# Kernel optimization log

Hardware: AMD Instinct MI355X
Metric: run time of the kernel (lower is better)

## Reference

```python
import jax, jax.numpy as jnp
import numpy as np

B, T, F, E = 256, 256, 8, 128
H = 2 * E  # hidden_dim = 2*embedding_dim = 256
NL = 5     # num_layers per LSTM stack


def setup_inputs() -> dict:
    key = jax.random.key(0)
    ks = jax.random.split(key, 9)
    s1 = 1.0 / np.sqrt(H)
    s2 = 1.0 / np.sqrt(E)
    u = lambda k, shape, s: jax.random.uniform(k, shape, jnp.float32, -s, s)
    return {
        "x": jax.random.normal(ks[0], (B, T, F), jnp.float32),
        # stack 1: input F -> hidden H, 5 layers. b = b_ih + b_hh combined.
        "w_ih0_1": u(ks[1], (4 * H, F), s1),
        "w_ihr_1": u(ks[2], (NL - 1, 4 * H, H), s1),
        "w_hh_1": u(ks[3], (NL, 4 * H, H), s1),
        "b_1": u(ks[4], (NL, 4 * H), s1),
        # stack 2: input H -> hidden E, 5 layers
        "w_ih0_2": u(ks[5], (4 * E, H), s2),
        "w_ihr_2": u(ks[6], (NL - 1, 4 * E, E), s2),
        "w_hh_2": u(ks[7], (NL, 4 * E, E), s2),
        "b_2": u(ks[8], (NL, 4 * E), s2),
    }


def _lstm_layer(x, w_ih, w_hh, b):
    """x: [B,T,D] -> (outputs [B,T,Hd], final hidden [B,Hd]). PyTorch gate order i,f,g,o."""
    Hd = w_hh.shape[-1]
    # precompute input contribution for all timesteps (the big GEMM)
    xg = jnp.einsum('btd,gd->tbg', x, w_ih) + b  # [T,B,4Hd]
    h0 = jnp.zeros((x.shape[0], Hd), x.dtype)

    def step(carry, xt):
        h, c = carry
        g = xt + h @ w_hh.T
        i, f, gg, o = jnp.split(g, 4, axis=-1)
        c = jax.nn.sigmoid(f) * c + jax.nn.sigmoid(i) * jnp.tanh(gg)
        h = jax.nn.sigmoid(o) * jnp.tanh(c)
        return (h, c), h

    (h, _), hs = jax.lax.scan(step, (h0, h0), xg)
    return jnp.swapaxes(hs, 0, 1), h


def _stack(x, w_ih0, w_ihr, w_hh, b):
    y, h = _lstm_layer(x, w_ih0, w_hh[0], b[0])
    for l in range(1, w_hh.shape[0]):
        y, h = _lstm_layer(y, w_ihr[l - 1], w_hh[l], b[l])
    return y, h


def reference(x, w_ih0_1, w_ihr_1, w_hh_1, b_1, w_ih0_2, w_ihr_2, w_hh_2, b_2):
    x = x.reshape(x.shape[0], T, F)
    y, _ = _stack(x, w_ih0_1, w_ihr_1, w_hh_1, b_1)   # [B,T,H]
    _, h = _stack(y, w_ih0_2, w_ihr_2, w_hh_2, b_2)   # h: [B,E] last layer final hidden
    return h
```

## Files before the change

### kernel.cpp

```cpp
#include <hip/hip_runtime.h>
#include <math.h>

typedef unsigned short u16;
typedef unsigned int   u32;
typedef unsigned long long u64;
typedef __bf16 bf16x8 __attribute__((ext_vector_type(8)));
typedef float  f32x4  __attribute__((ext_vector_type(4)));

#define BB 256
#define TT 256
#define HD 256
#define ED 128
#define DEPTH 4
#define NE 137

#define H_U32   (10 * DEPTH * BB * HD)
#define CTR_OFF H_U32
#define GRP_OFF (CTR_OFF + 512)
#define XP_OFF  (GRP_OFF + 640)
#define XP_U32  (BB * TT * 8)
#define WT_OFF  (XP_OFF + XP_U32)

__constant__ size_t g_woff[10] = {0ul,589824ul,1638400ul,2686976ul,3735552ul,
                                  4784128ul,5177344ul,5439488ul,5701632ul,5963776ul};
__constant__ int g_cb[11] = {0,73728,204800,335872,466944,598016,
                             647168,679936,712704,745472,778240};

__device__ __forceinline__ u16 f2bf_hi(float f) {
    u32 u = __float_as_uint(f);
    u32 r = (u + 0x7FFFu + ((u >> 16) & 1u)) >> 16;
    return (u16)r;
}
__device__ __forceinline__ float bf2f(u16 h) { return __uint_as_float(((u32)h) << 16); }
__device__ __forceinline__ float sigmoidf_(float v) { return 1.0f / (1.0f + expf(-v)); }

__global__ __launch_bounds__(256) void zero_state(u32* wsd) {
    const int n = XP_OFF;
    for (int i = blockIdx.x * blockDim.x + threadIdx.x; i < n; i += gridDim.x * blockDim.x)
        wsd[i] = 0u;
}

__global__ __launch_bounds__(256) void conv_x(const float* __restrict__ x, u32* __restrict__ wsd) {
    u32* xp = wsd + XP_OFF;
    for (int i = blockIdx.x * blockDim.x + threadIdx.x; i < XP_U32; i += gridDim.x * blockDim.x) {
        float v = x[i];
        u16 hi = f2bf_hi(v);
        u16 lo = f2bf_hi(v - bf2f(hi));
        xp[i] = (u32)hi | ((u32)lo << 16);
    }
}

__global__ __launch_bounds__(256) void conv_all(
    const float* __restrict__ w_ih0_1, const float* __restrict__ w_ihr_1,
    const float* __restrict__ w_hh_1,
    const float* __restrict__ w_ih0_2, const float* __restrict__ w_ihr_2,
    const float* __restrict__ w_hh_2,
    u32* __restrict__ wsd)
{
    __bf16* dst0 = (__bf16*)(wsd + WT_OFF);
    const int nch = 778240;
    for (int ci = blockIdx.x * blockDim.x + threadIdx.x; ci < nch;
         ci += gridDim.x * blockDim.x) {
        int l = 0;
        while (ci >= g_cb[l + 1]) ++l;
        int di = ci - g_cb[l];

        const int hd  = (l < 5) ? 256 : 128;
        const int din = (l == 0) ? 32 : ((l < 6) ? 256 : 128);
        const int xw  = (l == 0) ? 8 : din;
        const int Kp  = din + hd;
        const int nk  = Kp >> 5;

        const float *wih, *whh; int wihld, whhld;
        if (l == 0)      { wih = w_ih0_1;                                whh = w_hh_1;
                           wihld = 8;   whhld = 256; }
        else if (l < 5)  { wih = w_ihr_1 + (size_t)(l - 1) * 1024 * 256; whh = w_hh_1 + (size_t)l * 1024 * 256;
                           wihld = 256; whhld = 256; }
        else if (l == 5) { wih = w_ih0_2;                                whh = w_hh_2;
                           wihld = 256; whhld = 128; }
        else             { wih = w_ihr_2 + (size_t)(l - 6) * 512 * 128;  whh = w_hh_2 + (size_t)(l - 5) * 512 * 128;
                           wihld = 128; whhld = 128; }

        int lane = di & 63;
        int rem  = di >> 6;
        int kt   = rem % nk;
        int rem2 = rem / nk;
        int p    = rem2 & 1;
        int g    = (rem2 >> 1) & 3;
        int jt   = rem2 >> 3;
        int r15  = lane & 15, kq = lane >> 4;
        int row  = g * hd + jt * 16 + r15;

        bf16x8 o8;
        #pragma unroll
        for (int e = 0; e < 8; ++e) {
            int k = kt * 32 + kq * 8 + e;
            float v = 0.0f;
            if (k < xw) v = wih[(size_t)row * wihld + k];
            else if (k >= din && k < Kp) v = whh[(size_t)row * whhld + (k - din)];
            __bf16 h = (__bf16)v;
            o8[e] = p ? (__bf16)(v - (float)h) : h;
        }
        *(bf16x8*)(dst0 + g_woff[l] + (size_t)di * 8) = o8;
    }
}

__device__ __forceinline__ void unpack8(const uint4& a, const uint4& b, bf16x8& bh, bf16x8& bl) {
    union { u32 u[4]; bf16x8 v; } H, L;
    H.u[0] = (a.x & 0xFFFFu) | (a.y << 16);
    H.u[1] = (a.z & 0xFFFFu) | (a.w << 16);
    H.u[2] = (b.x & 0xFFFFu) | (b.y << 16);
    H.u[3] = (b.z & 0xFFFFu) | (b.w << 16);
    L.u[0] = (a.x >> 16) | (a.y & 0xFFFF0000u);
    L.u[1] = (a.z >> 16) | (a.w & 0xFFFF0000u);
    L.u[2] = (b.x >> 16) | (b.y & 0xFFFF0000u);
    L.u[3] = (b.z >> 16) | (b.w & 0xFFFF0000u);
    bh = H.v; bl = L.v;
}

template<int NKI, int NKT, bool ISL0>
__device__ void run_persist(int l, int bid, int xcd, int jt, int bt, int hd, u32 arr7,
    int nblkg, u32* __restrict__ gflg,
    const float* __restrict__ bias, u32* __restrict__ hbuf, u32* __restrict__ ctr,
    const u32* __restrict__ xp, float* __restrict__ out, const u16* __restrict__ A_sh)
{
    constexpr int DIN = NKI * 32;
    constexpr int RS  = (NKT < 4) ? NKT : 4;

    const int tid  = threadIdx.x;
    const int lane = tid & 63;
    const int wv   = tid >> 6;
    const int r15  = lane & 15;
    const int kqc  = lane >> 4;
    const int brow = bt * 128 + wv * 16 + r15;
    const int j0   = jt * 16 + kqc * 4;

    float bgr[4][4];
    #pragma unroll
    for (int g = 0; g < 4; ++g) {
        float4 v = *(const float4*)&bias[g * hd + j0];
        bgr[g][0] = v.x; bgr[g][1] = v.y; bgr[g][2] = v.z; bgr[g][3] = v.w;
    }

    int offH[4], offL[4];
    #pragma unroll
    for (int g = 0; g < 4; ++g) {
        offH[g] = (g * 2)     * NKT * 512 + lane * 8;
        offL[g] = (g * 2 + 1) * NKT * 512 + lane * 8;
    }

    float4 cv = make_float4(0.f, 0.f, 0.f, 0.f);
    const int lm = (l > 0) ? (l - 1) : 0;

    auto STEP = [&](int t) {
        const u32* hin   = hbuf + ((size_t)lm * DEPTH + (t & 3)) * (BB * HD);
        const u32* hprev = hbuf + ((size_t)l * DEPTH + ((t - 1) & 3)) * (BB * HD);
        u32*       hout  = hbuf + ((size_t)l * DEPTH + (t & 3)) * (BB * HD);

        auto ldB = [&](int kt, uint4& A, uint4& B) {
            if constexpr (ISL0) {
                if (kt == 0) {
                    if (kqc == 0) {
                        const uint4* p = (const uint4*)(xp + ((size_t)brow * TT + t) * 8);
                        A = p[0]; B = p[1];
                    } else { A = make_uint4(0,0,0,0); B = make_uint4(0,0,0,0); }
                } else {
                    const u32* p = hprev + (size_t)brow * HD + (kt * 32 - 32) + kqc * 8;
                    A = *(const uint4*)p; B = *(const uint4*)(p + 4);
                }
            } else {
                const int k0 = kt * 32 + kqc * 8;
                const u32* p = (k0 < DIN) ? (hin + (size_t)brow * HD + k0)
                                          : (hprev + (size_t)brow * HD + (k0 - DIN));
                A = *(const uint4*)p; B = *(const uint4*)(p + 4);
            }
        };

        f32x4 acc0 = {0.f,0.f,0.f,0.f}, acc1 = {0.f,0.f,0.f,0.f};
        f32x4 acc2 = {0.f,0.f,0.f,0.f}, acc3 = {0.f,0.f,0.f,0.f};

        uint4 ra[RS], rb[RS];
        #pragma unroll
        for (int i = 0; i < RS; ++i) ldB(i, ra[i], rb[i]);

        #pragma unroll
        for (int kt = 0; kt < NKT; ++kt) {
            bf16x8 bh, bl;
            unpack8(ra[kt % RS], rb[kt % RS], bh, bl);
            if (kt + RS < NKT) ldB(kt + RS, ra[kt % RS], rb[kt % RS]);

            const int kof = kt * 512;
            bf16x8 a0h = *(const bf16x8*)&A_sh[offH[0] + kof];
            bf16x8 a1h = *(const bf16x8*)&A_sh[offH[1] + kof];
            bf16x8 a2h = *(const bf16x8*)&A_sh[offH[2] + kof];
            bf16x8 a3h = *(const bf16x8*)&A_sh[offH[3] + kof];
            bf16x8 a0l = *(const bf16x8*)&A_sh[offL[0] + kof];
            bf16x8 a1l = *(const bf16x8*)&A_sh[offL[1] + kof];
            bf16x8 a2l = *(const bf16x8*)&A_sh[offL[2] + kof];
            bf16x8 a3l = *(const bf16x8*)&A_sh[offL[3] + kof];

            acc0 = __builtin_amdgcn_mfma_f32_16x16x32_bf16(a0h, bh, acc0, 0, 0, 0);
            acc1 = __builtin_amdgcn_mfma_f32_16x16x32_bf16(a1h, bh, acc1, 0, 0, 0);
            acc2 = __builtin_amdgcn_mfma_f32_16x16x32_bf16(a2h, bh, acc2, 0, 0, 0);
            acc3 = __builtin_amdgcn_mfma_f32_16x16x32_bf16(a3h, bh, acc3, 0, 0, 0);
            acc0 = __builtin_amdgcn_mfma_f32_16x16x32_bf16(a0h, bl, acc0, 0, 0, 0);
            acc1 = __builtin_amdgcn_mfma_f32_16x16x32_bf16(a1h, bl, acc1, 0, 0, 0);
            acc2 = __builtin_amdgcn_mfma_f32_16x16x32_bf16(a2h, bl, acc2, 0, 0, 0);
            acc3 = __builtin_amdgcn_mfma_f32_16x16x32_bf16(a3h, bl, acc3, 0, 0, 0);
            acc0 = __builtin_amdgcn_mfma_f32_16x16x32_bf16(a0l, bh, acc0, 0, 0, 0);
            acc1 = __builtin_amdgcn_mfma_f32_16x16x32_bf16(a1l, bh, acc1, 0, 0, 0);
            acc2 = __builtin_amdgcn_mfma_f32_16x16x32_bf16(a2l, bh, acc2, 0, 0, 0);
            acc3 = __builtin_amdgcn_mfma_f32_16x16x32_bf16(a3l, bh, acc3, 0, 0, 0);
        }

        float4 hv;
        {
            float i_, f_, g_, o_;
            i_ = sigmoidf_(acc0[0] + bgr[0][0]); f_ = sigmoidf_(acc1[0] + bgr[1][0]);
            g_ = tanhf   (acc2[0] + bgr[2][0]); o_ = sigmoidf_(acc3[0] + bgr[3][0]);
            cv.x = fmaf(f_, cv.x, i_ * g_); hv.x = o_ * tanhf(cv.x);
            i_ = sigmoidf_(acc0[1] + bgr[0][1]); f_ = sigmoidf_(acc1[1] + bgr[1][1]);
            g_ = tanhf   (acc2[1] + bgr[2][1]); o_ = sigmoidf_(acc3[1] + bgr[3][1]);
            cv.y = fmaf(f_, cv.y, i_ * g_); hv.y = o_ * tanhf(cv.y);
            i_ = sigmoidf_(acc0[2] + bgr[0][2]); f_ = sigmoidf_(acc1[2] + bgr[1][2]);
            g_ = tanhf   (acc2[2] + bgr[2][2]); o_ = sigmoidf_(acc3[2] + bgr[3][2]);
            cv.z = fmaf(f_, cv.z, i_ * g_); hv.z = o_ * tanhf(cv.z);
            i_ = sigmoidf_(acc0[3] + bgr[0][3]); f_ = sigmoidf_(acc1[3] + bgr[1][3]);
            g_ = tanhf   (acc2[3] + bgr[2][3]); o_ = sigmoidf_(acc3[3] + bgr[3][3]);
            cv.w = fmaf(f_, cv.w, i_ * g_); hv.w = o_ * tanhf(cv.w);
        }

        u32 pk0, pk1, pk2, pk3;
        {
            u16 h0 = f2bf_hi(hv.x); pk0 = (u32)h0 | ((u32)f2bf_hi(hv.x - bf2f(h0)) << 16);
            u16 h1 = f2bf_hi(hv.y); pk1 = (u32)h1 | ((u32)f2bf_hi(hv.y - bf2f(h1)) << 16);
            u16 h2 = f2bf_hi(hv.z); pk2 = (u32)h2 | ((u32)f2bf_hi(hv.z - bf2f(h2)) << 16);
            u16 h3 = f2bf_hi(hv.w); pk3 = (u32)h3 | ((u32)f2bf_hi(hv.w - bf2f(h3)) << 16);
        }
        u64* hp = (u64*)(hout + (size_t)brow * HD + j0);
        __hip_atomic_store(hp + 0, (u64)pk0 | ((u64)pk1 << 32), __ATOMIC_RELAXED, __HIP_MEMORY_SCOPE_AGENT);
        __hip_atomic_store(hp + 1, (u64)pk2 | ((u64)pk3 << 32), __ATOMIC_RELAXED, __HIP_MEMORY_SCOPE_AGENT);

        if (l == 9 && t == TT - 1)
            *(float4*)&out[(size_t)brow * ED + j0] = hv;
    };

    for (int E = 0; E < NE; ++E) {
        const int t0 = 2 * (E - l);
        if (t0 >= 0 && t0 < TT) {
            STEP(t0);
            __syncthreads();
            if (tid == 0)
                __hip_atomic_fetch_add(gflg, 1u, __ATOMIC_RELAXED, __HIP_MEMORY_SCOPE_AGENT);
        }
        const int t1 = t0 + 1;
        if (t1 >= 1 && t1 < TT) {
            if (tid == 0) {
                const u32 tg = (u32)nblkg * (u32)(E - l + 1);
                for (int it = 0; it < (1 << 20); ++it) {
                    if (__hip_atomic_load(gflg, __ATOMIC_RELAXED,
                                          __HIP_MEMORY_SCOPE_AGENT) >= tg) break;
                    __builtin_amdgcn_s_sleep(1);
                }
            }
            __syncthreads();
            STEP(t1);
        }

        __syncthreads();
        if (tid == 0) {
            __hip_atomic_fetch_add(&ctr[xcd * 32], 1u,
                                   __ATOMIC_RELAXED, __HIP_MEMORY_SCOPE_AGENT);
            const u32 w1 = (u32)(E + 1);
            if (bid == 0) {
                for (int it = 0; it < (1 << 22); ++it) {
                    bool ok = true;
                    #pragma unroll
                    for (int r = 0; r < 8; ++r) {
                        u32 tgt = ((r == 7) ? arr7 : 32u) * w1;
                        ok &= (__hip_atomic_load(&ctr[r * 32], __ATOMIC_RELAXED,
                                                 __HIP_MEMORY_SCOPE_AGENT) >= tgt);
                    }
                    if (ok) break;
                    __builtin_amdgcn_s_sleep(1);
                }
                __hip_atomic_store(&ctr[256], w1, __ATOMIC_RELAXED, __HIP_MEMORY_SCOPE_AGENT);
            } else {
                for (int it = 0; it < (1 << 22); ++it) {
                    if (__hip_atomic_load(&ctr[256], __ATOMIC_RELAXED,
                                          __HIP_MEMORY_SCOPE_AGENT) >= w1) break;
                    __builtin_amdgcn_s_sleep(1);
                }
            }
            __builtin_amdgcn_fence(__ATOMIC_ACQUIRE, "agent");
        }
        __syncthreads();
    }
}

__global__ __launch_bounds__(512, 2) void lstm_persist(
    const float* __restrict__ b_1, const float* __restrict__ b_2,
    u32* __restrict__ wsd, float* __restrict__ out)
{
    __shared__ __align__(16) u16 A_sh[65536];

    const int bid = blockIdx.x;
    const int xcd = bid & 7, slot = bid >> 3;
    int l, jt, bt;
    if (xcd < 5)      { l = xcd;               bt = slot >> 4;        jt = slot & 15; }
    else if (xcd == 5){ l = 5 + (slot >> 4);   bt = (slot >> 3) & 1;  jt = slot & 7; }
    else if (xcd == 6){ l = 7 + (slot >> 4);   bt = (slot >> 3) & 1;  jt = slot & 7; }
    else              { if (slot >= 16) return; l = 9; bt = slot >> 3; jt = slot & 7; }

    const int hd  = (l < 5) ? 256 : 128;
    const int din = (l == 0) ? 32 : ((l < 6) ? 256 : 128);
    const int nk  = (din + hd) >> 5;
    const float* bias = (l < 5) ? (b_1 + l * 1024) : (b_2 + (l - 5) * 512);
    const int nblkg = (l < 5) ? 32 : 16;

    u32* hbuf = wsd;
    u32* ctr  = wsd + CTR_OFF;
    u32* gflg = wsd + GRP_OFF + (size_t)(l * 2 + bt) * 32;
    const u32* xp = wsd + XP_OFF;
    const u16* wt = (const u16*)(wsd + WT_OFF);

    const int ng = (l < 5) ? 16 : 8;
    (void)nblkg;

    {
        const uint4* src = (const uint4*)(wt + g_woff[l] + (size_t)jt * 8 * nk * 512);
        uint4* dst = (uint4*)A_sh;
        const int n4 = nk * 512;
        for (int i = threadIdx.x; i < n4; i += 512) dst[i] = src[i];
    }
    __syncthreads();

    if (l == 0)
        run_persist<1, 9, true >(l, bid, xcd, jt, bt, hd, 16u, ng, gflg, bias, hbuf, ctr, xp, out, A_sh);
    else if (l < 5)
        run_persist<8, 16, false>(l, bid, xcd, jt, bt, hd, 16u, ng, gflg, bias, hbuf, ctr, xp, out, A_sh);
    else if (l == 5)
        run_persist<8, 12, false>(l, bid, xcd, jt, bt, hd, 16u, ng, gflg, bias, hbuf, ctr, xp, out, A_sh);
    else
        run_persist<4, 8, false>(l, bid, xcd, jt, bt, hd, 16u, ng, gflg, bias, hbuf, ctr, xp, out, A_sh);
}

extern "C" void kernel_launch(void* const* d_in, const int* in_sizes, int n_in,
                              void* d_out, int out_size, void* d_ws, size_t ws_size,
                              hipStream_t stream) {
    const float* x       = (const float*)d_in[0];
    const float* w_ih0_1 = (const float*)d_in[1];
    const float* w_ihr_1 = (const float*)d_in[2];
    const float* w_hh_1  = (const float*)d_in[3];
    const float* b_1     = (const float*)d_in[4];
    const float* w_ih0_2 = (const float*)d_in[5];
    const float* w_ihr_2 = (const float*)d_in[6];
    const float* w_hh_2  = (const float*)d_in[7];
    const float* b_2     = (const float*)d_in[8];
    u32*   wsd = (u32*)d_ws;
    float* out = (float*)d_out;

    hipLaunchKernelGGL(zero_state, dim3(1024), dim3(256), 0, stream, wsd);
    hipLaunchKernelGGL(conv_all, dim3(1024), dim3(256), 0, stream,
                       w_ih0_1, w_ihr_1, w_hh_1, w_ih0_2, w_ihr_2, w_hh_2, wsd);
    hipLaunchKernelGGL(conv_x, dim3(256), dim3(256), 0, stream, x, wsd);
    hipLaunchKernelGGL(lstm_persist, dim3(256), dim3(512), 0, stream,
                       b_1, b_2, wsd, out);
}
```

Before: 2.998 ms.

## Process four timesteps per global epoch and keep part of the weights in registers

The wavefront schedule changes from two timesteps per grid-wide barrier to four, with intra-group flag waits between steps. This halves the number of epochs and deepens the hidden-state ring buffer to eight slots. The high-precision halves of gates 0 and 1 now live in registers, loaded directly from global memory, so the shared-memory weight slice shrinks to six sub-blocks and fewer LDS reads are issued per k-tile. The prefetch depth drops from four to three to make room. The cost is heavy register pressure from NKT-sized register arrays, which may spill or limit occupancy, and longer per-epoch dependency chains across layers.

Result: slower. 3.197 ms (+6.6%).

```diff
diff --git a/kernel.cpp b/kernel.cpp
--- a/kernel.cpp
+++ b/kernel.cpp
@@ -11,8 +11,8 @@
 #define TT 256
 #define HD 256
 #define ED 128
-#define DEPTH 4
-#define NE 137
+#define DEPTH 8
+#define NE 73
 
 #define H_U32   (10 * DEPTH * BB * HD)
 #define CTR_OFF H_U32
@@ -120,12 +120,13 @@
 
 template<int NKI, int NKT, bool ISL0>
 __device__ void run_persist(int l, int bid, int xcd, int jt, int bt, int hd, u32 arr7,
-    int nblkg, u32* __restrict__ gflg,
+    int ng, u32* __restrict__ gflg,
     const float* __restrict__ bias, u32* __restrict__ hbuf, u32* __restrict__ ctr,
-    const u32* __restrict__ xp, float* __restrict__ out, const u16* __restrict__ A_sh)
+    const u32* __restrict__ xp, float* __restrict__ out,
+    const u16* __restrict__ A_sh, const u16* __restrict__ wslice)
 {
     constexpr int DIN = NKI * 32;
-    constexpr int RS  = (NKT < 4) ? NKT : 4;
+    constexpr int RS  = (NKT < 3) ? NKT : 3;
 
     const int tid  = threadIdx.x;
     const int lane = tid & 63;
@@ -135,6 +136,13 @@
     const int brow = bt * 128 + wv * 16 + r15;
     const int j0   = jt * 16 + kqc * 4;
 
+    bf16x8 A_reg[2][NKT];
+    #pragma unroll
+    for (int g = 0; g < 2; ++g)
+        #pragma unroll
+        for (int kt = 0; kt < NKT; ++kt)
+            A_reg[g][kt] = *(const bf16x8*)(wslice + ((size_t)(g * 2) * NKT + kt) * 512 + lane * 8);
+
     float bgr[4][4];
     #pragma unroll
     for (int g = 0; g < 4; ++g) {
@@ -142,20 +150,19 @@
         bgr[g][0] = v.x; bgr[g][1] = v.y; bgr[g][2] = v.z; bgr[g][3] = v.w;
     }
 
-    int offH[4], offL[4];
+    int loOff[4];
     #pragma unroll
-    for (int g = 0; g < 4; ++g) {
-        offH[g] = (g * 2)     * NKT * 512 + lane * 8;
-        offL[g] = (g * 2 + 1) * NKT * 512 + lane * 8;
-    }
+    for (int g = 0; g < 4; ++g) loOff[g] = (g * NKT) * 512 + lane * 8;
+    const int hi2Off = (4 * NKT) * 512 + lane * 8;
+    const int hi3Off = (5 * NKT) * 512 + lane * 8;
 
     float4 cv = make_float4(0.f, 0.f, 0.f, 0.f);
     const int lm = (l > 0) ? (l - 1) : 0;
 
     auto STEP = [&](int t) {
-        const u32* hin   = hbuf + ((size_t)lm * DEPTH + (t & 3)) * (BB * HD);
-        const u32* hprev = hbuf + ((size_t)l * DEPTH + ((t - 1) & 3)) * (BB * HD);
-        u32*       hout  = hbuf + ((size_t)l * DEPTH + (t & 3)) * (BB * HD);
+        const u32* hin   = hbuf + ((size_t)lm * DEPTH + (t & 7)) * (BB * HD);
+        const u32* hprev = hbuf + ((size_t)l * DEPTH + ((t - 1) & 7)) * (BB * HD);
+        u32*       hout  = hbuf + ((size_t)l * DEPTH + (t & 7)) * (BB * HD);
 
         auto ldB = [&](int kt, uint4& A, uint4& B) {
             if constexpr (ISL0) {
@@ -190,14 +197,14 @@
             if (kt + RS < NKT) ldB(kt + RS, ra[kt % RS], rb[kt % RS]);
 
             const int kof = kt * 512;
-            bf16x8 a0h = *(const bf16x8*)&A_sh[offH[0] + kof];
-            bf16x8 a1h = *(const bf16x8*)&A_sh[offH[1] + kof];
-            bf16x8 a2h = *(const bf16x8*)&A_sh[offH[2] + kof];
-            bf16x8 a3h = *(const bf16x8*)&A_sh[offH[3] + kof];
-            bf16x8 a0l = *(const bf16x8*)&A_sh[offL[0] + kof];
-            bf16x8 a1l = *(const bf16x8*)&A_sh[offL[1] + kof];
-            bf16x8 a2l = *(const bf16x8*)&A_sh[offL[2] + kof];
-            bf16x8 a3l = *(const bf16x8*)&A_sh[offL[3] + kof];
+            bf16x8 a0h = A_reg[0][kt];
+            bf16x8 a1h = A_reg[1][kt];
+            bf16x8 a2h = *(const bf16x8*)&A_sh[hi2Off + kof];
+            bf16x8 a3h = *(const bf16x8*)&A_sh[hi3Off + kof];
+            bf16x8 a0l = *(const bf16x8*)&A_sh[loOff[0] + kof];
+            bf16x8 a1l = *(const bf16x8*)&A_sh[loOff[1] + kof];
+            bf16x8 a2l = *(const bf16x8*)&A_sh[loOff[2] + kof];
+            bf16x8 a3l = *(const bf16x8*)&A_sh[loOff[3] + kof];
 
             acc0 = __builtin_amdgcn_mfma_f32_16x16x32_bf16(a0h, bh, acc0, 0, 0, 0);
             acc1 = __builtin_amdgcn_mfma_f32_16x16x32_bf16(a1h, bh, acc1, 0, 0, 0);
@@ -246,25 +253,29 @@
     };
 
     for (int E = 0; E < NE; ++E) {
-        const int t0 = 2 * (E - l);
-        if (t0 >= 0 && t0 < TT) {
-            STEP(t0);
-            __syncthreads();
-            if (tid == 0)
-                __hip_atomic_fetch_add(gflg, 1u, __ATOMIC_RELAXED, __HIP_MEMORY_SCOPE_AGENT);
-        }
-        const int t1 = t0 + 1;
-        if (t1 >= 1 && t1 < TT) {
-            if (tid == 0) {
-                const u32 tg = (u32)nblkg * (u32)(E - l + 1);
-                for (int it = 0; it < (1 << 20); ++it) {
-                    if (__hip_atomic_load(gflg, __ATOMIC_RELAXED,
-                                          __HIP_MEMORY_SCOPE_AGENT) >= tg) break;
-                    __builtin_amdgcn_s_sleep(1);
+        const int ep = E - l;
+        if (ep >= 0 && ep < 64) {
+            #pragma unroll 1
+            for (int i = 0; i < 4; ++i) {
+                const int t = 4 * ep + i;
+                if (i > 0) {
+                    if (tid == 0) {
+                        const u32 tg = (u32)ng * (u32)(3 * ep + i);
+                        for (int it = 0; it < (1 << 20); ++it) {
+                            if (__hip_atomic_load(gflg, __ATOMIC_RELAXED,
+                                                  __HIP_MEMORY_SCOPE_AGENT) >= tg) break;
+                            __builtin_amdgcn_s_sleep(1);
+                        }
+                    }
+                    __syncthreads();
+                }
+                STEP(t);
+                if (i < 3) {
+                    __syncthreads();
+                    if (tid == 0)
+                        __hip_atomic_fetch_add(gflg, 1u, __ATOMIC_RELAXED, __HIP_MEMORY_SCOPE_AGENT);
                 }
             }
-            __syncthreads();
-            STEP(t1);
         }
 
         __syncthreads();
@@ -302,7 +313,7 @@
     const float* __restrict__ b_1, const float* __restrict__ b_2,
     u32* __restrict__ wsd, float* __restrict__ out)
 {
-    __shared__ __align__(16) u16 A_sh[65536];
+    __shared__ __align__(16) u16 A_sh[49152];
 
     const int bid = blockIdx.x;
     const int xcd = bid & 7, slot = bid >> 3;
@@ -316,33 +327,36 @@
     const int din = (l == 0) ? 32 : ((l < 6) ? 256 : 128);
     const int nk  = (din + hd) >> 5;
     const float* bias = (l < 5) ? (b_1 + l * 1024) : (b_2 + (l - 5) * 512);
-    const int nblkg = (l < 5) ? 32 : 16;
 
     u32* hbuf = wsd;
     u32* ctr  = wsd + CTR_OFF;
     u32* gflg = wsd + GRP_OFF + (size_t)(l * 2 + bt) * 32;
     const u32* xp = wsd + XP_OFF;
     const u16* wt = (const u16*)(wsd + WT_OFF);
+    const u16* wslice = wt + g_woff[l] + (size_t)jt * 8 * nk * 512;
 
     const int ng = (l < 5) ? 16 : 8;
-    (void)nblkg;
 
     {
-        const uint4* src = (const uint4*)(wt + g_woff[l] + (size_t)jt * 8 * nk * 512);
-        uint4* dst = (uint4*)A_sh;
-        const int n4 = nk * 512;
-        for (int i = threadIdx.x; i < n4; i += 512) dst[i] = src[i];
+        const uint4* src4 = (const uint4*)wslice;
+        uint4* dst4 = (uint4*)A_sh;
+        const int spc = nk * 64;
+        for (int i = threadIdx.x; i < 6 * spc; i += 512) {
+            int d = i / spc, r = i - d * spc;
+            int s = (d < 4) ? (d * 2 + 1) : ((d == 4) ? 4 : 6);
+            dst4[i] = src4[s * spc + r];
+        }
     }
     __syncthreads();
 
     if (l == 0)
-        run_persist<1, 9, true >(l, bid, xcd, jt, bt, hd, 16u, ng, gflg, bias, hbuf, ctr, xp, out, A_sh);
+        run_persist<1, 9, true >(l, bid, xcd, jt, bt, hd, 16u, ng, gflg, bias, hbuf, ctr, xp, out, A_sh, wslice);
     else if (l < 5)
-        run_persist<8, 16, false>(l, bid, xcd, jt, bt, hd, 16u, ng, gflg, bias, hbuf, ctr, xp, out, A_sh);
+        run_persist<8, 16, false>(l, bid, xcd, jt, bt, hd, 16u, ng, gflg, bias, hbuf, ctr, xp, out, A_sh, wslice);
     else if (l == 5)
-        run_persist<8, 12, false>(l, bid, xcd, jt, bt, hd, 16u, ng, gflg, bias, hbuf, ctr, xp, out, A_sh);
+        run_persist<8, 12, false>(l, bid, xcd, jt, bt, hd, 16u, ng, gflg, bias, hbuf, ctr, xp, out, A_sh, wslice);
     else
-        run_persist<4, 8, false>(l, bid, xcd, jt, bt, hd, 16u, ng, gflg, bias, hbuf, ctr, xp, out, A_sh);
+        run_persist<4, 8, false>(l, bid, xcd, jt, bt, hd, 16u, ng, gflg, bias, hbuf, ctr, xp, out, A_sh, wslice);
 }
 
 extern "C" void kernel_launch(void* const* d_in, const int* in_sizes, int n_in,
```

## Switch recurrent GEMM to 32x32x16 MFMA with gate-interleaved weight layout

Applied to the files above, without the earlier changes.

Replaces the four 16x16x32 MFMA accumulators per gate with 32x32x16 MFMAs whose output rows interleave the four gates for 8 hidden units. The weight repacking kernel is changed so each 32-row tile holds i,f,g,o for one hidden unit. Each wave now covers 32 batch rows and 8 hidden units, and two accumulators alternate over K steps to break MFMA dependency chains. This cuts LDS A-fragment loads and per-step instruction count, at the cost of larger accumulator register use, narrower scalar 32-bit h stores and a changed load prefetch depth.

New measurement: 5.244 ms. 1.75x slower.

```diff
diff --git a/kernel.cpp b/kernel.cpp
--- a/kernel.cpp
+++ b/kernel.cpp
@@ -6,6 +6,7 @@
 typedef unsigned long long u64;
 typedef __bf16 bf16x8 __attribute__((ext_vector_type(8)));
 typedef float  f32x4  __attribute__((ext_vector_type(4)));
+typedef float  f32x16 __attribute__((ext_vector_type(16)));
 
 #define BB 256
 #define TT 256
@@ -69,7 +70,7 @@
         const int din = (l == 0) ? 32 : ((l < 6) ? 256 : 128);
         const int xw  = (l == 0) ? 8 : din;
         const int Kp  = din + hd;
-        const int nk  = Kp >> 5;
+        const int NK2 = Kp >> 4;
 
         const float *wih, *whh; int wihld, whhld;
         if (l == 0)      { wih = w_ih0_1;                                whh = w_hh_1;
@@ -83,18 +84,20 @@
 
         int lane = di & 63;
         int rem  = di >> 6;
-        int kt   = rem % nk;
-        int rem2 = rem / nk;
+        int s    = rem % NK2;
+        int rem2 = rem / NK2;
         int p    = rem2 & 1;
-        int g    = (rem2 >> 1) & 3;
-        int jt   = rem2 >> 3;
-        int r15  = lane & 15, kq = lane >> 4;
-        int row  = g * hd + jt * 16 + r15;
+        int jh   = (rem2 >> 1) & 1;
+        int jt   = rem2 >> 2;
+        int r31  = lane & 31;
+        int jloc = r31 >> 2, gate = r31 & 3;
+        int kh   = (lane >> 5) * 8;
+        int row  = gate * hd + jt * 16 + jh * 8 + jloc;
 
         bf16x8 o8;
         #pragma unroll
         for (int e = 0; e < 8; ++e) {
-            int k = kt * 32 + kq * 8 + e;
+            int k = s * 16 + kh + e;
             float v = 0.0f;
             if (k < xw) v = wih[(size_t)row * wihld + k];
             else if (k >= din && k < Kp) v = whh[(size_t)row * whhld + (k - din)];
@@ -118,38 +121,37 @@
     bh = H.v; bl = L.v;
 }
 
-template<int NKI, int NKT, bool ISL0>
+template<int DIN16, int NK2, bool ISL0>
 __device__ void run_persist(int l, int bid, int xcd, int jt, int bt, int hd, u32 arr7,
-    int nblkg, u32* __restrict__ gflg,
+    int ng, u32* __restrict__ gflg,
     const float* __restrict__ bias, u32* __restrict__ hbuf, u32* __restrict__ ctr,
     const u32* __restrict__ xp, float* __restrict__ out, const u16* __restrict__ A_sh)
 {
-    constexpr int DIN = NKI * 32;
-    constexpr int RS  = (NKT < 4) ? NKT : 4;
+    constexpr int DIN = DIN16 * 16;
+    constexpr int RS  = (NK2 < 3) ? NK2 : 3;
 
     const int tid  = threadIdx.x;
     const int lane = tid & 63;
     const int wv   = tid >> 6;
-    const int r15  = lane & 15;
-    const int kqc  = lane >> 4;
-    const int brow = bt * 128 + wv * 16 + r15;
-    const int j0   = jt * 16 + kqc * 4;
+    const int bq   = wv >> 1;
+    const int jh   = wv & 1;
+    const int r31  = lane & 31;
+    const int hi   = lane >> 5;
+    const int kh   = hi * 8;
+    const int b    = bt * 128 + bq * 32 + r31;
+    const int jBase = jt * 16 + jh * 8;
+
+    const int hiOff = ((jh * 2 + 0) * NK2) * 512 + lane * 8;
+    const int loOff = ((jh * 2 + 1) * NK2) * 512 + lane * 8;
 
     float bgr[4][4];
     #pragma unroll
-    for (int g = 0; g < 4; ++g) {
-        float4 v = *(const float4*)&bias[g * hd + j0];
-        bgr[g][0] = v.x; bgr[g][1] = v.y; bgr[g][2] = v.z; bgr[g][3] = v.w;
-    }
-
-    int offH[4], offL[4];
-    #pragma unroll
-    for (int g = 0; g < 4; ++g) {
-        offH[g] = (g * 2)     * NKT * 512 + lane * 8;
-        offL[g] = (g * 2 + 1) * NKT * 512 + lane * 8;
-    }
-
-    float4 cv = make_float4(0.f, 0.f, 0.f, 0.f);
+    for (int q = 0; q < 4; ++q)
+        #pragma unroll
+        for (int g = 0; g < 4; ++g)
+            bgr[q][g] = bias[g * hd + jBase + 2 * q + hi];
+
+    f32x4 cv = {0.f, 0.f, 0.f, 0.f};
     const int lm = (l > 0) ? (l - 1) : 0;
 
     auto STEP = [&](int t) {
@@ -157,92 +159,70 @@
         const u32* hprev = hbuf + ((size_t)l * DEPTH + ((t - 1) & 3)) * (BB * HD);
         u32*       hout  = hbuf + ((size_t)l * DEPTH + (t & 3)) * (BB * HD);
 
-        auto ldB = [&](int kt, uint4& A, uint4& B) {
+        auto ldB = [&](int s, uint4& A, uint4& B) {
             if constexpr (ISL0) {
-                if (kt == 0) {
-                    if (kqc == 0) {
-                        const uint4* p = (const uint4*)(xp + ((size_t)brow * TT + t) * 8);
+                if (s == 0) {
+                    if (hi == 0) {
+                        const uint4* p = (const uint4*)(xp + ((size_t)b * TT + t) * 8);
                         A = p[0]; B = p[1];
                     } else { A = make_uint4(0,0,0,0); B = make_uint4(0,0,0,0); }
+                } else if (s == 1) {
+                    A = make_uint4(0,0,0,0); B = make_uint4(0,0,0,0);
                 } else {
-                    const u32* p = hprev + (size_t)brow * HD + (kt * 32 - 32) + kqc * 8;
+                    const u32* p = hprev + (size_t)b * HD + (s * 16 - 32) + kh;
                     A = *(const uint4*)p; B = *(const uint4*)(p + 4);
                 }
             } else {
-                const int k0 = kt * 32 + kqc * 8;
-                const u32* p = (k0 < DIN) ? (hin + (size_t)brow * HD + k0)
-                                          : (hprev + (size_t)brow * HD + (k0 - DIN));
+                const int k0 = s * 16 + kh;
+                const u32* p = (k0 < DIN) ? (hin + (size_t)b * HD + k0)
+                                          : (hprev + (size_t)b * HD + (k0 - DIN));
                 A = *(const uint4*)p; B = *(const uint4*)(p + 4);
             }
         };
 
-        f32x4 acc0 = {0.f,0.f,0.f,0.f}, acc1 = {0.f,0.f,0.f,0.f};
-        f32x4 acc2 = {0.f,0.f,0.f,0.f}, acc3 = {0.f,0.f,0.f,0.f};
+        f32x16 accA, accB;
+        #pragma unroll
+        for (int i = 0; i < 16; ++i) { accA[i] = 0.f; accB[i] = 0.f; }
 
         uint4 ra[RS], rb[RS];
         #pragma unroll
         for (int i = 0; i < RS; ++i) ldB(i, ra[i], rb[i]);
 
         #pragma unroll
-        for (int kt = 0; kt < NKT; ++kt) {
+        for (int s = 0; s < NK2; ++s) {
             bf16x8 bh, bl;
-            unpack8(ra[kt % RS], rb[kt % RS], bh, bl);
-            if (kt + RS < NKT) ldB(kt + RS, ra[kt % RS], rb[kt % RS]);
-
-            const int kof = kt * 512;
-            bf16x8 a0h = *(const bf16x8*)&A_sh[offH[0] + kof];
-            bf16x8 a1h = *(const bf16x8*)&A_sh[offH[1] + kof];
-            bf16x8 a2h = *(const bf16x8*)&A_sh[offH[2] + kof];
-            bf16x8 a3h = *(const bf16x8*)&A_sh[offH[3] + kof];
-            bf16x8 a0l = *(const bf16x8*)&A_sh[offL[0] + kof];
-            bf16x8 a1l = *(const bf16x8*)&A_sh[offL[1] + kof];
-            bf16x8 a2l = *(const bf16x8*)&A_sh[offL[2] + kof];
-            bf16x8 a3l = *(const bf16x8*)&A_sh[offL[3] + kof];
-
-            acc0 = __builtin_amdgcn_mfma_f32_16x16x32_bf16(a0h, bh, acc0, 0, 0, 0);
-            acc1 = __builtin_amdgcn_mfma_f32_16x16x32_bf16(a1h, bh, acc1, 0, 0, 0);
-            acc2 = __builtin_amdgcn_mfma_f32_16x16x32_bf16(a2h, bh, acc2, 0, 0, 0);
-            acc3 = __builtin_amdgcn_mfma_f32_16x16x32_bf16(a3h, bh, acc3, 0, 0, 0);
-            acc0 = __builtin_amdgcn_mfma_f32_16x16x32_bf16(a0h, bl, acc0, 0, 0, 0);
-            acc1 = __builtin_amdgcn_mfma_f32_16x16x32_bf16(a1h, bl, acc1, 0, 0, 0);
-            acc2 = __builtin_amdgcn_mfma_f32_16x16x32_bf16(a2h, bl, acc2, 0, 0, 0);
-            acc3 = __builtin_amdgcn_mfma_f32_16x16x32_bf16(a3h, bl, acc3, 0, 0, 0);
-            acc0 = __builtin_amdgcn_mfma_f32_16x16x32_bf16(a0l, bh, acc0, 0, 0, 0);
-            acc1 = __builtin_amdgcn_mfma_f32_16x16x32_bf16(a1l, bh, acc1, 0, 0, 0);
-            acc2 = __builtin_amdgcn_mfma_f32_16x16x32_bf16(a2l, bh, acc2, 0, 0, 0);
-            acc3 = __builtin_amdgcn_mfma_f32_16x16x32_bf16(a3l, bh, acc3, 0, 0, 0);
-        }
-
-        float4 hv;
-        {
-            float i_, f_, g_, o_;
-            i_ = sigmoidf_(acc0[0] + bgr[0][0]); f_ = sigmoidf_(acc1[0] + bgr[1][0]);
-            g_ = tanhf   (acc2[0] + bgr[2][0]); o_ = sigmoidf_(acc3[0] + bgr[3][0]);
-            cv.x = fmaf(f_, cv.x, i_ * g_); hv.x = o_ * tanhf(cv.x);
-            i_ = sigmoidf_(acc0[1] + bgr[0][1]); f_ = sigmoidf_(acc1[1] + bgr[1][1]);
-            g_ = tanhf   (acc2[1] + bgr[2][1]); o_ = sigmoidf_(acc3[1] + bgr[3][1]);
-            cv.y = fmaf(f_, cv.y, i_ * g_); hv.y = o_ * tanhf(cv.y);
-            i_ = sigmoidf_(acc0[2] + bgr[0][2]); f_ = sigmoidf_(acc1[2] + bgr[1][2]);
-            g_ = tanhf   (acc2[2] + bgr[2][2]); o_ = sigmoidf_(acc3[2] + bgr[3][2]);
-            cv.z = fmaf(f_, cv.z, i_ * g_); hv.z = o_ * tanhf(cv.z);
-            i_ = sigmoidf_(acc0[3] + bgr[0][3]); f_ = sigmoidf_(acc1[3] + bgr[1][3]);
-            g_ = tanhf   (acc2[3] + bgr[2][3]); o_ = sigmoidf_(acc3[3] + bgr[3][3]);
-            cv.w = fmaf(f_, cv.w, i_ * g_); hv.w = o_ * tanhf(cv.w);
-        }
-
-        u32 pk0, pk1, pk2, pk3;
-        {
-            u16 h0 = f2bf_hi(hv.x); pk0 = (u32)h0 | ((u32)f2bf_hi(hv.x - bf2f(h0)) << 16);
-            u16 h1 = f2bf_hi(hv.y); pk1 = (u32)h1 | ((u32)f2bf_hi(hv.y - bf2f(h1)) << 16);
-            u16 h2 = f2bf_hi(hv.z); pk2 = (u32)h2 | ((u32)f2bf_hi(hv.z - bf2f(h2)) << 16);
-            u16 h3 = f2bf_hi(hv.w); pk3 = (u32)h3 | ((u32)f2bf_hi(hv.w - bf2f(h3)) << 16);
-        }
-        u64* hp = (u64*)(hout + (size_t)brow * HD + j0);
-        __hip_atomic_store(hp + 0, (u64)pk0 | ((u64)pk1 << 32), __ATOMIC_RELAXED, __HIP_MEMORY_SCOPE_AGENT);
-        __hip_atomic_store(hp + 1, (u64)pk2 | ((u64)pk3 << 32), __ATOMIC_RELAXED, __HIP_MEMORY_SCOPE_AGENT);
-
-        if (l == 9 && t == TT - 1)
-            *(float4*)&out[(size_t)brow * ED + j0] = hv;
+            unpack8(ra[s % RS], rb[s % RS], bh, bl);
+            if (s + RS < NK2) ldB(s + RS, ra[s % RS], rb[s % RS]);
+
+            bf16x8 ah = *(const bf16x8*)&A_sh[hiOff + s * 512];
+            bf16x8 al = *(const bf16x8*)&A_sh[loOff + s * 512];
+
+            if (s & 1) {
+                accB = __builtin_amdgcn_mfma_f32_32x32x16_bf16(ah, bh, accB, 0, 0, 0);
+                accB = __builtin_amdgcn_mfma_f32_32x32x16_bf16(ah, bl, accB, 0, 0, 0);
+                accB = __builtin_amdgcn_mfma_f32_32x32x16_bf16(al, bh, accB, 0, 0, 0);
+            } else {
+                accA = __builtin_amdgcn_mfma_f32_32x32x16_bf16(ah, bh, accA, 0, 0, 0);
+                accA = __builtin_amdgcn_mfma_f32_32x32x16_bf16(ah, bl, accA, 0, 0, 0);
+                accA = __builtin_amdgcn_mfma_f32_32x32x16_bf16(al, bh, accA, 0, 0, 0);
+            }
+        }
+
+        #pragma unroll
+        for (int q = 0; q < 4; ++q) {
+            float i_ = sigmoidf_(accA[q*4+0] + accB[q*4+0] + bgr[q][0]);
+            float f_ = sigmoidf_(accA[q*4+1] + accB[q*4+1] + bgr[q][1]);
+            float g_ = tanhf   (accA[q*4+2] + accB[q*4+2] + bgr[q][2]);
+            float o_ = sigmoidf_(accA[q*4+3] + accB[q*4+3] + bgr[q][3]);
+            cv[q] = fmaf(f_, cv[q], i_ * g_);
+            float hv = o_ * tanhf(cv[q]);
+            u16 h0 = f2bf_hi(hv);
+            u32 pk = (u32)h0 | ((u32)f2bf_hi(hv - bf2f(h0)) << 16);
+            const int j = jBase + 2 * q + hi;
+            __hip_atomic_store(hout + (size_t)b * HD + j, pk,
+                               __ATOMIC_RELAXED, __HIP_MEMORY_SCOPE_AGENT);
+            if (l == 9 && t == TT - 1) out[(size_t)b * ED + j] = hv;
+        }
     };
 
     for (int E = 0; E < NE; ++E) {
@@ -256,7 +236,7 @@
         const int t1 = t0 + 1;
         if (t1 >= 1 && t1 < TT) {
             if (tid == 0) {
-                const u32 tg = (u32)nblkg * (u32)(E - l + 1);
+                const u32 tg = (u32)ng * (u32)(E - l + 1);
                 for (int it = 0; it < (1 << 20); ++it) {
                     if (__hip_atomic_load(gflg, __ATOMIC_RELAXED,
                                           __HIP_MEMORY_SCOPE_AGENT) >= tg) break;
@@ -314,9 +294,8 @@
 
     const int hd  = (l < 5) ? 256 : 128;
     const int din = (l == 0) ? 32 : ((l < 6) ? 256 : 128);
-    const int nk  = (din + hd) >> 5;
+    const int NK2 = (din + hd) >> 4;
     const float* bias = (l < 5) ? (b_1 + l * 1024) : (b_2 + (l - 5) * 512);
-    const int nblkg = (l < 5) ? 32 : 16;
 
     u32* hbuf = wsd;
     u32* ctr  = wsd + CTR_OFF;
@@ -325,24 +304,23 @@
     const u16* wt = (const u16*)(wsd + WT_OFF);
 
     const int ng = (l < 5) ? 16 : 8;
-    (void)nblkg;
 
     {
-        const uint4* src = (const uint4*)(wt + g_woff[l] + (size_t)jt * 8 * nk * 512);
+        const uint4* src = (const uint4*)(wt + g_woff[l] + (size_t)jt * 4 * NK2 * 512);
         uint4* dst = (uint4*)A_sh;
-        const int n4 = nk * 512;
+        const int n4 = NK2 * 256;
         for (int i = threadIdx.x; i < n4; i += 512) dst[i] = src[i];
     }
     __syncthreads();
 
     if (l == 0)
-        run_persist<1, 9, true >(l, bid, xcd, jt, bt, hd, 16u, ng, gflg, bias, hbuf, ctr, xp, out, A_sh);
+        run_persist<2, 18, true >(l, bid, xcd, jt, bt, hd, 16u, ng, gflg, bias, hbuf, ctr, xp, out, A_sh);
     else if (l < 5)
+        run_persist<16, 32, false>(l, bid, xcd, jt, bt, hd, 16u, ng, gflg, bias, hbuf, ctr, xp, out, A_sh);
+    else if (l == 5)
+        run_persist<16, 24, false>(l, bid, xcd, jt, bt, hd, 16u, ng, gflg, bias, hbuf, ctr, xp, out, A_sh);
+    else
         run_persist<8, 16, false>(l, bid, xcd, jt, bt, hd, 16u, ng, gflg, bias, hbuf, ctr, xp, out, A_sh);
-    else if (l == 5)
-        run_persist<8, 12, false>(l, bid, xcd, jt, bt, hd, 16u, ng, gflg, bias, hbuf, ctr, xp, out, A_sh);
-    else
-        run_persist<4, 8, false>(l, bid, xcd, jt, bt, hd, 16u, ng, gflg, bias, hbuf, ctr, xp, out, A_sh);
 }
 
 extern "C" void kernel_launch(void* const* d_in, const int* in_sizes, int n_in,
```

## Split hidden-state ring into hi/lo planes and process four timesteps per epoch

Applied to the files above, without the earlier changes.

Stores the bf16 hi and lo parts of hidden states and the input in separate planes, so loads feed the MFMA operands directly with no unpack shuffles. The ring depth goes from 4 to 8 and each wavefront epoch now covers four timesteps instead of two. This halves the number of global cross-layer barrier epochs (from 137 to 73) and relies more on per-group flags inside an epoch. The cost is more ring memory and longer pipeline fill and drain across layers.

Result: faster. 2.890 ms (-3.6%).

```diff
diff --git a/kernel.cpp b/kernel.cpp
--- a/kernel.cpp
+++ b/kernel.cpp
@@ -11,15 +11,16 @@
 #define TT 256
 #define HD 256
 #define ED 128
-#define DEPTH 4
-#define NE 137
-
-#define H_U32   (10 * DEPTH * BB * HD)
-#define CTR_OFF H_U32
+#define DEPTH 8
+#define NE 73
+
+#define HRING   (10 * DEPTH * BB * HD / 2)
+#define CTR_OFF (2 * HRING)
 #define GRP_OFF (CTR_OFF + 512)
-#define XP_OFF  (GRP_OFF + 640)
-#define XP_U32  (BB * TT * 8)
-#define WT_OFF  (XP_OFF + XP_U32)
+#define XP_U32  (BB * TT * 8 / 2)
+#define XPH_OFF (GRP_OFF + 640)
+#define XPL_OFF (XPH_OFF + XP_U32)
+#define WT_OFF  (XPL_OFF + XP_U32)
 
 __constant__ size_t g_woff[10] = {0ul,589824ul,1638400ul,2686976ul,3735552ul,
                                   4784128ul,5177344ul,5439488ul,5701632ul,5963776ul};
@@ -35,18 +36,20 @@
 __device__ __forceinline__ float sigmoidf_(float v) { return 1.0f / (1.0f + expf(-v)); }
 
 __global__ __launch_bounds__(256) void zero_state(u32* wsd) {
-    const int n = XP_OFF;
+    const int n = XPH_OFF;
     for (int i = blockIdx.x * blockDim.x + threadIdx.x; i < n; i += gridDim.x * blockDim.x)
         wsd[i] = 0u;
 }
 
 __global__ __launch_bounds__(256) void conv_x(const float* __restrict__ x, u32* __restrict__ wsd) {
-    u32* xp = wsd + XP_OFF;
-    for (int i = blockIdx.x * blockDim.x + threadIdx.x; i < XP_U32; i += gridDim.x * blockDim.x) {
+    u16* xph = (u16*)(wsd + XPH_OFF);
+    u16* xpl = (u16*)(wsd + XPL_OFF);
+    const int n = BB * TT * 8;
+    for (int i = blockIdx.x * blockDim.x + threadIdx.x; i < n; i += gridDim.x * blockDim.x) {
         float v = x[i];
         u16 hi = f2bf_hi(v);
-        u16 lo = f2bf_hi(v - bf2f(hi));
-        xp[i] = (u32)hi | ((u32)lo << 16);
+        xph[i] = hi;
+        xpl[i] = f2bf_hi(v - bf2f(hi));
     }
 }
 
@@ -105,27 +108,19 @@
     }
 }
 
-__device__ __forceinline__ void unpack8(const uint4& a, const uint4& b, bf16x8& bh, bf16x8& bl) {
-    union { u32 u[4]; bf16x8 v; } H, L;
-    H.u[0] = (a.x & 0xFFFFu) | (a.y << 16);
-    H.u[1] = (a.z & 0xFFFFu) | (a.w << 16);
-    H.u[2] = (b.x & 0xFFFFu) | (b.y << 16);
-    H.u[3] = (b.z & 0xFFFFu) | (b.w << 16);
-    L.u[0] = (a.x >> 16) | (a.y & 0xFFFF0000u);
-    L.u[1] = (a.z >> 16) | (a.w & 0xFFFF0000u);
-    L.u[2] = (b.x >> 16) | (b.y & 0xFFFF0000u);
-    L.u[3] = (b.z >> 16) | (b.w & 0xFFFF0000u);
-    bh = H.v; bl = L.v;
-}
-
 template<int NKI, int NKT, bool ISL0>
 __device__ void run_persist(int l, int bid, int xcd, int jt, int bt, int hd, u32 arr7,
-    int nblkg, u32* __restrict__ gflg,
-    const float* __restrict__ bias, u32* __restrict__ hbuf, u32* __restrict__ ctr,
-    const u32* __restrict__ xp, float* __restrict__ out, const u16* __restrict__ A_sh)
+    int ng, u32* __restrict__ gflg,
+    const float* __restrict__ bias, u32* __restrict__ wsd, u32* __restrict__ ctr,
+    float* __restrict__ out, const u16* __restrict__ A_sh)
 {
     constexpr int DIN = NKI * 32;
     constexpr int RS  = (NKT < 4) ? NKT : 4;
+
+    u16* hhi = (u16*)wsd;
+    u16* hlo = (u16*)(wsd + HRING);
+    const u16* xph = (const u16*)(wsd + XPH_OFF);
+    const u16* xpl = (const u16*)(wsd + XPL_OFF);
 
     const int tid  = threadIdx.x;
     const int lane = tid & 63;
@@ -153,26 +148,29 @@
     const int lm = (l > 0) ? (l - 1) : 0;
 
     auto STEP = [&](int t) {
-        const u32* hin   = hbuf + ((size_t)lm * DEPTH + (t & 3)) * (BB * HD);
-        const u32* hprev = hbuf + ((size_t)l * DEPTH + ((t - 1) & 3)) * (BB * HD);
-        u32*       hout  = hbuf + ((size_t)l * DEPTH + (t & 3)) * (BB * HD);
-
-        auto ldB = [&](int kt, uint4& A, uint4& B) {
+        const size_t sIn   = ((size_t)lm * DEPTH + (t & 7)) * (BB * HD);
+        const size_t sPrev = ((size_t)l * DEPTH + ((t - 1) & 7)) * (BB * HD);
+        const size_t sOut  = ((size_t)l * DEPTH + (t & 7)) * (BB * HD);
+
+        auto ldB = [&](int kt, uint4& H4, uint4& L4) {
             if constexpr (ISL0) {
                 if (kt == 0) {
                     if (kqc == 0) {
-                        const uint4* p = (const uint4*)(xp + ((size_t)brow * TT + t) * 8);
-                        A = p[0]; B = p[1];
-                    } else { A = make_uint4(0,0,0,0); B = make_uint4(0,0,0,0); }
+                        const size_t xo = ((size_t)brow * TT + t) * 8;
+                        H4 = *(const uint4*)(xph + xo);
+                        L4 = *(const uint4*)(xpl + xo);
+                    } else { H4 = make_uint4(0,0,0,0); L4 = make_uint4(0,0,0,0); }
                 } else {
-                    const u32* p = hprev + (size_t)brow * HD + (kt * 32 - 32) + kqc * 8;
-                    A = *(const uint4*)p; B = *(const uint4*)(p + 4);
+                    const size_t o = sPrev + (size_t)brow * HD + (kt * 32 - 32) + kqc * 8;
+                    H4 = *(const uint4*)(hhi + o);
+                    L4 = *(const uint4*)(hlo + o);
                 }
             } else {
                 const int k0 = kt * 32 + kqc * 8;
-                const u32* p = (k0 < DIN) ? (hin + (size_t)brow * HD + k0)
-                                          : (hprev + (size_t)brow * HD + (k0 - DIN));
-                A = *(const uint4*)p; B = *(const uint4*)(p + 4);
+                const size_t o = (k0 < DIN) ? (sIn + (size_t)brow * HD + k0)
+                                            : (sPrev + (size_t)brow * HD + (k0 - DIN));
+                H4 = *(const uint4*)(hhi + o);
+                L4 = *(const uint4*)(hlo + o);
             }
         };
 
@@ -185,8 +183,9 @@
 
         #pragma unroll
         for (int kt = 0; kt < NKT; ++kt) {
-            bf16x8 bh, bl;
-            unpack8(ra[kt % RS], rb[kt % RS], bh, bl);
+            union { uint4 u; bf16x8 v; } BH, BL;
+            BH.u = ra[kt % RS]; BL.u = rb[kt % RS];
+            bf16x8 bh = BH.v, bl = BL.v;
             if (kt + RS < NKT) ldB(kt + RS, ra[kt % RS], rb[kt % RS]);
 
             const int kof = kt * 512;
@@ -230,41 +229,44 @@
             cv.w = fmaf(f_, cv.w, i_ * g_); hv.w = o_ * tanhf(cv.w);
         }
 
-        u32 pk0, pk1, pk2, pk3;
-        {
-            u16 h0 = f2bf_hi(hv.x); pk0 = (u32)h0 | ((u32)f2bf_hi(hv.x - bf2f(h0)) << 16);
-            u16 h1 = f2bf_hi(hv.y); pk1 = (u32)h1 | ((u32)f2bf_hi(hv.y - bf2f(h1)) << 16);
-            u16 h2 = f2bf_hi(hv.z); pk2 = (u32)h2 | ((u32)f2bf_hi(hv.z - bf2f(h2)) << 16);
-            u16 h3 = f2bf_hi(hv.w); pk3 = (u32)h3 | ((u32)f2bf_hi(hv.w - bf2f(h3)) << 16);
-        }
-        u64* hp = (u64*)(hout + (size_t)brow * HD + j0);
-        __hip_atomic_store(hp + 0, (u64)pk0 | ((u64)pk1 << 32), __ATOMIC_RELAXED, __HIP_MEMORY_SCOPE_AGENT);
-        __hip_atomic_store(hp + 1, (u64)pk2 | ((u64)pk3 << 32), __ATOMIC_RELAXED, __HIP_MEMORY_SCOPE_AGENT);
+        u16 h0 = f2bf_hi(hv.x), h1 = f2bf_hi(hv.y), h2 = f2bf_hi(hv.z), h3 = f2bf_hi(hv.w);
+        u64 hiP = (u64)h0 | ((u64)h1 << 16) | ((u64)h2 << 32) | ((u64)h3 << 48);
+        u64 loP = (u64)f2bf_hi(hv.x - bf2f(h0)) |
+                  ((u64)f2bf_hi(hv.y - bf2f(h1)) << 16) |
+                  ((u64)f2bf_hi(hv.z - bf2f(h2)) << 32) |
+                  ((u64)f2bf_hi(hv.w - bf2f(h3)) << 48);
+        const size_t ho = sOut + (size_t)brow * HD + j0;
+        __hip_atomic_store((u64*)(hhi + ho), hiP, __ATOMIC_RELAXED, __HIP_MEMORY_SCOPE_AGENT);
+        __hip_atomic_store((u64*)(hlo + ho), loP, __ATOMIC_RELAXED, __HIP_MEMORY_SCOPE_AGENT);
 
         if (l == 9 && t == TT - 1)
             *(float4*)&out[(size_t)brow * ED + j0] = hv;
     };
 
     for (int E = 0; E < NE; ++E) {
-        const int t0 = 2 * (E - l);
-        if (t0 >= 0 && t0 < TT) {
-            STEP(t0);
-            __syncthreads();
-            if (tid == 0)
-                __hip_atomic_fetch_add(gflg, 1u, __ATOMIC_RELAXED, __HIP_MEMORY_SCOPE_AGENT);
-        }
-        const int t1 = t0 + 1;
-        if (t1 >= 1 && t1 < TT) {
-            if (tid == 0) {
-                const u32 tg = (u32)nblkg * (u32)(E - l + 1);
-                for (int it = 0; it < (1 << 20); ++it) {
-                    if (__hip_atomic_load(gflg, __ATOMIC_RELAXED,
-                                          __HIP_MEMORY_SCOPE_AGENT) >= tg) break;
-                    __builtin_amdgcn_s_sleep(1);
+        const int ep = E - l;
+        if (ep >= 0 && ep < 64) {
+            #pragma unroll 1
+            for (int i = 0; i < 4; ++i) {
+                const int t = 4 * ep + i;
+                if (i > 0) {
+                    if (tid == 0) {
+                        const u32 tg = (u32)ng * (u32)(3 * ep + i);
+                        for (int it = 0; it < (1 << 20); ++it) {
+                            if (__hip_atomic_load(gflg, __ATOMIC_RELAXED,
+                                                  __HIP_MEMORY_SCOPE_AGENT) >= tg) break;
+                            __builtin_amdgcn_s_sleep(1);
+                        }
+                    }
+                    __syncthreads();
+                }
+                STEP(t);
+                if (i < 3) {
+                    __syncthreads();
+                    if (tid == 0)
+                        __hip_atomic_fetch_add(gflg, 1u, __ATOMIC_RELAXED, __HIP_MEMORY_SCOPE_AGENT);
                 }
             }
-            __syncthreads();
-            STEP(t1);
         }
 
         __syncthreads();
@@ -316,16 +318,12 @@
     const int din = (l == 0) ? 32 : ((l < 6) ? 256 : 128);
     const int nk  = (din + hd) >> 5;
     const float* bias = (l < 5) ? (b_1 + l * 1024) : (b_2 + (l - 5) * 512);
-    const int nblkg = (l < 5) ? 32 : 16;
-
-    u32* hbuf = wsd;
+
     u32* ctr  = wsd + CTR_OFF;
     u32* gflg = wsd + GRP_OFF + (size_t)(l * 2 + bt) * 32;
-    const u32* xp = wsd + XP_OFF;
     const u16* wt = (const u16*)(wsd + WT_OFF);
 
     const int ng = (l < 5) ? 16 : 8;
-    (void)nblkg;
 
     {
         const uint4* src = (const uint4*)(wt + g_woff[l] + (size_t)jt * 8 * nk * 512);
@@ -336,13 +334,13 @@
     __syncthreads();
 
     if (l == 0)
-        run_persist<1, 9, true >(l, bid, xcd, jt, bt, hd, 16u, ng, gflg, bias, hbuf, ctr, xp, out, A_sh);
+        run_persist<1, 9, true >(l, bid, xcd, jt, bt, hd, 16u, ng, gflg, bias, wsd, ctr, out, A_sh);
     else if (l < 5)
-        run_persist<8, 16, false>(l, bid, xcd, jt, bt, hd, 16u, ng, gflg, bias, hbuf, ctr, xp, out, A_sh);
+        run_persist<8, 16, false>(l, bid, xcd, jt, bt, hd, 16u, ng, gflg, bias, wsd, ctr, out, A_sh);
     else if (l == 5)
-        run_persist<8, 12, false>(l, bid, xcd, jt, bt, hd, 16u, ng, gflg, bias, hbuf, ctr, xp, out, A_sh);
+        run_persist<8, 12, false>(l, bid, xcd, jt, bt, hd, 16u, ng, gflg, bias, wsd, ctr, out, A_sh);
     else
-        run_persist<4, 8, false>(l, bid, xcd, jt, bt, hd, 16u, ng, gflg, bias, hbuf, ctr, xp, out, A_sh);
+        run_persist<4, 8, false>(l, bid, xcd, jt, bt, hd, 16u, ng, gflg, bias, wsd, ctr, out, A_sh);
 }
 
 extern "C" void kernel_launch(void* const* d_in, const int* in_sizes, int n_in,
```
